# Optimization experiments

Hardware: AMD Instinct MI355X
Metric: run time of the kernel (lower is better)

Reference implementation:

```python
import jax, jax.numpy as jnp
import numpy as np

B, S, D = 1, 2048, 2048
HQ, HKV, HD = 32, 4, 128
E, K, F = 8, 2, 768
EPS = 1e-6
ROPE_THETA = 1000000.0


def rmsnorm(x, scale, eps=EPS):
    var = jnp.mean(jnp.square(x), axis=-1, keepdims=True)
    return x * jax.lax.rsqrt(var + eps) * scale


def rotate_half(x):
    h = x.shape[-1] // 2
    return jnp.concatenate([-x[..., h:], x[..., :h]], axis=-1)


def rope_cos_sin(seq_len, head_dim, dtype=jnp.float32):
    inv_freq = 1.0 / (ROPE_THETA ** (jnp.arange(0, head_dim, 2, dtype=jnp.float32) / head_dim))
    angles = jnp.arange(seq_len, dtype=jnp.float32)[:, None] * inv_freq[None, :]  # (S, HD/2)
    emb = jnp.concatenate([angles, angles], axis=-1)  # (S, HD)
    return jnp.cos(emb).astype(dtype), jnp.sin(emb).astype(dtype)


def setup_inputs() -> dict:
    key = jax.random.key(0)
    ks = jax.random.split(key, 16)
    s = lambda i, shape, scale: jax.random.normal(ks[i], shape, dtype=jnp.float32) * scale
    inp = {
        "hidden_states": s(0, (B, S, D), 1.0),
        "ln1_scale": jnp.ones((D,), jnp.float32),
        "ln2_scale": jnp.ones((D,), jnp.float32),
        "Wq": s(1, (D, HQ * HD), 0.02),
        "Wk": s(2, (D, HKV * HD), 0.02),
        "Wv": s(3, (D, HKV * HD), 0.02),
        "Wo": s(4, (HQ * HD, D), 0.02),
        "q_norm_scale": jnp.ones((HD,), jnp.float32),
        "k_norm_scale": jnp.ones((HD,), jnp.float32),
        "router_W": s(5, (D, E), 0.02),
        "up_W": s(6, (E, D, F), 0.02),
        "up_b": jnp.zeros((E, F), jnp.float32),
        "down_W": s(7, (E, F, D), 0.02),
        "down_b": jnp.zeros((E, D), jnp.float32),
    }
    return inp


def reference(hidden_states, ln1_scale, ln2_scale, Wq, Wk, Wv, Wo,
              q_norm_scale, k_norm_scale, router_W, up_W, up_b, down_W, down_b):
    b, s_len, d = hidden_states.shape
    # ---- pre-norm + self-attention ----
    residual = hidden_states
    x = rmsnorm(hidden_states, ln1_scale)
    q = (x @ Wq).reshape(b, s_len, HQ, HD)
    k = (x @ Wk).reshape(b, s_len, HKV, HD)
    v = (x @ Wv).reshape(b, s_len, HKV, HD)
    q = rmsnorm(q, q_norm_scale)
    k = rmsnorm(k, k_norm_scale)
    cos, sin = rope_cos_sin(s_len, HD, q.dtype)
    cos = cos[None, :, None, :]
    sin = sin[None, :, None, :]
    q = q * cos + rotate_half(q) * sin
    k = k * cos + rotate_half(k) * sin
    g = HQ // HKV
    k = jnp.repeat(k, g, axis=2)  # (b, s, HQ, HD)
    v = jnp.repeat(v, g, axis=2)
    scores = jnp.einsum('bqhd,bkhd->bhqk', q, k) / jnp.sqrt(jnp.asarray(HD, q.dtype))
    causal = jnp.tril(jnp.ones((s_len, s_len), bool))
    scores = jnp.where(causal[None, None], scores, jnp.asarray(-1e9, scores.dtype))
    probs = jax.nn.softmax(scores, axis=-1)
    attn = jnp.einsum('bhqk,bkhd->bqhd', probs, v).reshape(b, s_len, HQ * HD)
    attn_out = attn @ Wo
    hidden = residual + attn_out
    # ---- pre-norm + dense-all-experts MoE ----
    residual = hidden
    xf = rmsnorm(hidden, ln2_scale).reshape(-1, d)  # (T, D)
    router_logits = xf @ router_W  # (T, E)
    routing_weights = jax.nn.softmax(router_logits, axis=-1)
    gating_weights, selected = jax.lax.top_k(routing_weights, K)  # (T, K)
    gating_weights = gating_weights / jnp.sum(gating_weights, axis=-1, keepdims=True)
    expert_mask = jax.nn.one_hot(selected, E, dtype=gating_weights.dtype)  # (T, K, E)
    h = jax.nn.silu(jnp.einsum('td,edf->tef', xf, up_W) + up_b[None])  # (T, E, F)
    expert_outputs = jnp.einsum('tef,efd->ted', h, down_W) + down_b[None]  # (T, E, D)
    weighted = jnp.einsum('tke,ted->tkd', expert_mask, expert_outputs)  # (T, K, D)
    moe_out = jnp.sum(weighted * gating_weights[..., None], axis=1).reshape(b, s_len, d)
    hidden = residual + moe_out
    # ---- load balancing auxiliary loss (no attention mask path) ----
    expert_usage = jnp.mean(jnp.mean(expert_mask, axis=0), axis=0) * E  # (E,)
    su = jnp.sum(expert_usage)
    aux_loss = su * su / (E * E)
    return hidden, router_logits, aux_loss
```

## Files before the change

### kernel.cpp

```cpp
#include <hip/hip_runtime.h>
#include <cmath>

typedef __bf16 bf16_t;
typedef __bf16 bf16x8 __attribute__((ext_vector_type(8)));
typedef __bf16 bf16x4 __attribute__((ext_vector_type(4)));
typedef float  f32x4  __attribute__((ext_vector_type(4)));

#define SLEN 2048
#define DMOD 2048
#define NHQ  32
#define NHKV 4
#define HD   128
#define NQC  4096
#define NKVC 512
#define NQKVC 5120
#define NEXP 8
#define NF   768

#define KSTR 136
#define VSTR 72
#define PSTR 72

__device__ __forceinline__ float wredsum(float v) {
#pragma unroll
  for (int off = 32; off > 0; off >>= 1) v += __shfl_xor(v, off);
  return v;
}

__device__ __forceinline__ void gll16(const bf16_t* g, bf16_t* l) {
  __builtin_amdgcn_global_load_lds((const __attribute__((address_space(1))) void*)g,
                                   (__attribute__((address_space(3))) void*)l, 16, 0, 0);
}

__global__ void rope_table_k(float* __restrict__ cosT, float* __restrict__ sinT) {
  int idx = blockIdx.x * 256 + threadIdx.x;
  if (idx >= SLEN * 64) return;
  int t = idx >> 6, j = idx & 63;
  double inv = exp(-0.2158673524681918 * (double)j);
  double ang = (double)t * inv;
  cosT[idx] = (float)cos(ang);
  sinT[idx] = (float)sin(ang);
}

__global__ __launch_bounds__(256) void transpose_split2_k(const float* __restrict__ in,
                                                          bf16_t* __restrict__ outH,
                                                          bf16_t* __restrict__ outL,
                                                          int R, int C) {
  __shared__ float tile[32][33];
  int tx = threadIdx.x, ty = threadIdx.y;
  int c0 = blockIdx.x * 32, r0 = blockIdx.y * 32;
#pragma unroll
  for (int i = 0; i < 4; i++)
    tile[ty + i * 8][tx] = in[(size_t)(r0 + ty + i * 8) * C + c0 + tx];
  __syncthreads();
#pragma unroll
  for (int i = 0; i < 4; i++) {
    int c = c0 + ty + i * 8;
    int r = r0 + tx;
    float w = tile[tx][ty + i * 8];
    bf16_t hi = (bf16_t)w;
    bf16_t lo = (bf16_t)(w - (float)hi);
    size_t o = (size_t)c * R + r;
    outH[o] = hi;
    outL[o] = lo;
  }
}

__global__ __launch_bounds__(256) void transpose_plain_k(const float* __restrict__ in,
                                                         bf16_t* __restrict__ out,
                                                         int R, int C) {
  __shared__ float tile[32][33];
  int b = blockIdx.z;
  const float* inb = in + (size_t)b * R * C;
  bf16_t* outb = out + (size_t)b * R * C;
  int tx = threadIdx.x, ty = threadIdx.y;
  int c0 = blockIdx.x * 32, r0 = blockIdx.y * 32;
#pragma unroll
  for (int i = 0; i < 4; i++)
    tile[ty + i * 8][tx] = inb[(size_t)(r0 + ty + i * 8) * C + c0 + tx];
  __syncthreads();
#pragma unroll
  for (int i = 0; i < 4; i++) {
    int c = c0 + ty + i * 8;
    int r = r0 + tx;
    outb[(size_t)c * R + r] = (bf16_t)tile[tx][ty + i * 8];
  }
}

__global__ __launch_bounds__(256) void rmsnorm1_k(const float* __restrict__ hs,
                                                  const float* __restrict__ sc,
                                                  bf16_t* __restrict__ xnH,
                                                  bf16_t* __restrict__ xnL) {
  const int t = blockIdx.x;
  const float* row = hs + (size_t)t * DMOD;
  const int tid = threadIdx.x;
  const int i0 = tid * 8;
  float4 a = *(const float4*)(row + i0);
  float4 b = *(const float4*)(row + i0 + 4);
  float x[8] = {a.x, a.y, a.z, a.w, b.x, b.y, b.z, b.w};
  float ss = 0.f;
#pragma unroll
  for (int j = 0; j < 8; j++) ss += x[j] * x[j];
  ss = wredsum(ss);
  __shared__ float red[4];
  if ((tid & 63) == 0) red[tid >> 6] = ss;
  __syncthreads();
  float rn = rsqrtf((red[0] + red[1] + red[2] + red[3]) * (1.f / 2048.f) + 1e-6f);
#pragma unroll
  for (int j = 0; j < 8; j++) {
    float v = x[j] * rn * sc[i0 + j];
    bf16_t hi = (bf16_t)v;
    bf16_t lo = (bf16_t)(v - (float)hi);
    xnH[(size_t)t * DMOD + i0 + j] = hi;
    xnL[(size_t)t * DMOD + i0 + j] = lo;
  }
}

template <bool RESID>
__global__ __launch_bounds__(256) void gemm_split128_k(const bf16_t* __restrict__ Ah,
                                                       const bf16_t* __restrict__ Al,
                                                       int lda,
                                                       const bf16_t* __restrict__ Bh,
                                                       const bf16_t* __restrict__ Bl,
                                                       int ldb, int K,
                                                       const float* __restrict__ resid,
                                                       float* __restrict__ C, int ldc) {
  __shared__ bf16_t AsH[2][128][32], AsL[2][128][32], BsH[2][128][32], BsL[2][128][32];
  const int t = threadIdx.x;
  const int w = t >> 6, lane = t & 63;
  const int m16 = lane & 15, quad = lane >> 4;
  const int nwg = gridDim.x * gridDim.y;
  const int flat = blockIdx.y * gridDim.x + blockIdx.x;
  int tile = flat;
  if ((nwg & 7) == 0) tile = (flat & 7) * (nwg >> 3) + (flat >> 3);
  const int bx = tile % gridDim.x, by = tile / gridDim.x;
  const int m0 = by * 128, n0 = bx * 128;
  const int wm = (w & 1) * 64, wn = (w >> 1) * 64;
  f32x4 acc[4][4];
#pragma unroll
  for (int i = 0; i < 4; i++)
#pragma unroll
    for (int j = 0; j < 4; j++) acc[i][j] = (f32x4){0.f, 0.f, 0.f, 0.f};

  const int srow = t >> 2;
  const int scol = (t & 3) * 8;
  const int lw = w * 512;
  const bf16_t* gAh0 = Ah + (size_t)(m0 + srow) * lda + scol;
  const bf16_t* gAh1 = Ah + (size_t)(m0 + 64 + srow) * lda + scol;
  const bf16_t* gAl0 = Al + (size_t)(m0 + srow) * lda + scol;
  const bf16_t* gAl1 = Al + (size_t)(m0 + 64 + srow) * lda + scol;
  const bf16_t* gBh0 = Bh + (size_t)(n0 + srow) * ldb + scol;
  const bf16_t* gBh1 = Bh + (size_t)(n0 + 64 + srow) * ldb + scol;
  const bf16_t* gBl0 = Bl + (size_t)(n0 + srow) * ldb + scol;
  const bf16_t* gBl1 = Bl + (size_t)(n0 + 64 + srow) * ldb + scol;

  auto stage = [&](int buf, int k0) {
    gll16(gAh0 + k0, &AsH[buf][0][0] + lw);
    gll16(gAh1 + k0, &AsH[buf][0][0] + 2048 + lw);
    gll16(gAl0 + k0, &AsL[buf][0][0] + lw);
    gll16(gAl1 + k0, &AsL[buf][0][0] + 2048 + lw);
    gll16(gBh0 + k0, &BsH[buf][0][0] + lw);
    gll16(gBh1 + k0, &BsH[buf][0][0] + 2048 + lw);
    gll16(gBl0 + k0, &BsL[buf][0][0] + lw);
    gll16(gBl1 + k0, &BsL[buf][0][0] + 2048 + lw);
  };

  stage(0, 0);
  int cur = 0;
  for (int k0 = 32; k0 <= K; k0 += 32) {
    if (k0 < K) {
      stage(cur ^ 1, k0);
      asm volatile("s_waitcnt vmcnt(8)" ::: "memory");
    } else {
      asm volatile("s_waitcnt vmcnt(0)" ::: "memory");
    }
    __builtin_amdgcn_sched_barrier(0);
    __builtin_amdgcn_s_barrier();
    __builtin_amdgcn_sched_barrier(0);
    bf16x8 a_h[4], a_l[4];
#pragma unroll
    for (int mt = 0; mt < 4; mt++) {
      a_h[mt] = *(const bf16x8*)(&AsH[cur][wm + mt * 16 + m16][quad * 8]);
      a_l[mt] = *(const bf16x8*)(&AsL[cur][wm + mt * 16 + m16][quad * 8]);
    }
#pragma unroll
    for (int nt = 0; nt < 4; nt++) {
      bf16x8 b_h = *(const bf16x8*)(&BsH[cur][wn + nt * 16 + m16][quad * 8]);
      bf16x8 b_l = *(const bf16x8*)(&BsL[cur][wn + nt * 16 + m16][quad * 8]);
#pragma unroll
      for (int mt = 0; mt < 4; mt++) {
        acc[mt][nt] = __builtin_amdgcn_mfma_f32_16x16x32_bf16(a_h[mt], b_h, acc[mt][nt], 0, 0, 0);
        acc[mt][nt] = __builtin_amdgcn_mfma_f32_16x16x32_bf16(a_l[mt], b_h, acc[mt][nt], 0, 0, 0);
        acc[mt][nt] = __builtin_amdgcn_mfma_f32_16x16x32_bf16(a_h[mt], b_l, acc[mt][nt], 0, 0, 0);
      }
    }
    __builtin_amdgcn_sched_barrier(0);
    __builtin_amdgcn_s_barrier();
    __builtin_amdgcn_sched_barrier(0);
    cur ^= 1;
  }
#pragma unroll
  for (int mt = 0; mt < 4; mt++)
#pragma unroll
    for (int r = 0; r < 4; r++) {
      const size_t row = m0 + wm + mt * 16 + quad * 4 + r;
#pragma unroll
      for (int nt = 0; nt < 4; nt++) {
        const size_t idx = row * ldc + n0 + wn + nt * 16 + m16;
        if (RESID) C[idx] = acc[mt][nt][r] + resid[idx];
        else       C[idx] = acc[mt][nt][r];
      }
    }
}

template <class AROW>
__device__ __forceinline__ void gemm_core(AROW getA, const bf16_t* __restrict__ Bt, int ldb,
                                          int n0, int K, f32x4 acc[4]) {
  __shared__ bf16_t As[64][32];
  __shared__ bf16_t Bs[64][32];
  const int t = threadIdx.x;
  const int wave = t >> 6, lane = t & 63;
  const int m16 = lane & 15, quad = lane >> 4;
  const int sr = t >> 2, sc = (t & 3) << 3;
  const bf16_t* __restrict__ arow = getA(sr);
  const bf16_t* __restrict__ brow = Bt + (size_t)(n0 + sr) * ldb;
  for (int k0 = 0; k0 < K; k0 += 32) {
    __syncthreads();
    *(uint4*)(&As[sr][sc]) = *(const uint4*)(arow + k0 + sc);
    *(uint4*)(&Bs[sr][sc]) = *(const uint4*)(brow + k0 + sc);
    __syncthreads();
    bf16x8 af = *(const bf16x8*)(&As[wave * 16 + m16][quad * 8]);
#pragma unroll
    for (int nt = 0; nt < 4; nt++) {
      bf16x8 bfr = *(const bf16x8*)(&Bs[nt * 16 + m16][quad * 8]);
      acc[nt] = __builtin_amdgcn_mfma_f32_16x16x32_bf16(af, bfr, acc[nt], 0, 0, 0);
    }
  }
}

__global__ __launch_bounds__(128) void qknorm_rope_k(float* __restrict__ qkv,
                                                     const float* __restrict__ qsc,
                                                     const float* __restrict__ ksc,
                                                     const float* __restrict__ cosT,
                                                     const float* __restrict__ sinT) {
  const int t = blockIdx.x;
  const int hh = blockIdx.y;
  const bool isq = hh < NHQ;
  float* ptr = qkv + (size_t)t * NQKVC + (isq ? hh * HD : NQC + (hh - NHQ) * HD);
  const int i = threadIdx.x;
  float x = ptr[i];
  float ss = x * x;
  ss = wredsum(ss);
  __shared__ float red2[2];
  __shared__ float xs[128];
  if ((i & 63) == 0) red2[i >> 6] = ss;
  __syncthreads();
  float rn = rsqrtf((red2[0] + red2[1]) * (1.f / 128.f) + 1e-6f);
  float xn = x * rn * (isq ? qsc[i] : ksc[i]);
  xs[i] = xn;
  __syncthreads();
  int j = i & 63;
  float c = cosT[t * 64 + j];
  float s = sinT[t * 64 + j];
  float rot = (i < 64) ? -xs[i + 64] : xs[i - 64];
  ptr[i] = xn * c + rot * s;
}

__global__ __launch_bounds__(256) void kprep_k(const float* __restrict__ qkv,
                                               bf16_t* __restrict__ Kh,
                                               bf16_t* __restrict__ Kl) {
  const int gid = blockIdx.x * 256 + threadIdx.x;
  const int tok = gid >> 6;
  const int c = (gid & 63) * 8;
  const int hk = c >> 7, d = c & 127;
  const float* p = qkv + (size_t)tok * NQKVC + NQC + c;
  float4 a = *(const float4*)p;
  float4 b = *(const float4*)(p + 4);
  float xv[8] = {a.x, a.y, a.z, a.w, b.x, b.y, b.z, b.w};
  bf16x8 hv, lv;
#pragma unroll
  for (int j = 0; j < 8; j++) {
    bf16_t hi = (bf16_t)xv[j];
    hv[j] = hi;
    lv[j] = (bf16_t)(xv[j] - (float)hi);
  }
  const size_t o = ((size_t)hk * SLEN + tok) * HD + d;
  *(bf16x8*)(Kh + o) = hv;
  *(bf16x8*)(Kl + o) = lv;
}

__global__ __launch_bounds__(256) void vprep_k(const float* __restrict__ qkv,
                                               bf16_t* __restrict__ Vh,
                                               bf16_t* __restrict__ Vl) {
  __shared__ float tile[32][33];
  const int hk = blockIdx.z;
  const int tx = threadIdx.x, ty = threadIdx.y;
  const int t0 = blockIdx.x * 32, d0 = blockIdx.y * 32;
#pragma unroll
  for (int i = 0; i < 4; i++)
    tile[ty + i * 8][tx] =
        qkv[(size_t)(t0 + ty + i * 8) * NQKVC + NQC + NKVC + hk * HD + d0 + tx];
  __syncthreads();
#pragma unroll
  for (int i = 0; i < 4; i++) {
    int d = d0 + ty + i * 8;
    int tk = t0 + tx;
    float wv = tile[tx][ty + i * 8];
    bf16_t hi = (bf16_t)wv;
    size_t o = ((size_t)hk * HD + d) * SLEN + tk;
    Vh[o] = hi;
    Vl[o] = (bf16_t)(wv - (float)hi);
  }
}

__global__ __launch_bounds__(256) void attn_mfma_k(const float* __restrict__ qkv,
                                                   const bf16_t* __restrict__ Kph,
                                                   const bf16_t* __restrict__ Kpl,
                                                   const bf16_t* __restrict__ Vph,
                                                   const bf16_t* __restrict__ Vpl,
                                                   bf16_t* __restrict__ attnH,
                                                   bf16_t* __restrict__ attnL) {
  const int bx = blockIdx.x;
  const int hh = blockIdx.y;
  const int hk = hh >> 3;
  __shared__ bf16_t sK[2][64][KSTR];
  __shared__ bf16_t sV[2][128][VSTR];
  const int t = threadIdx.x;
  const int w = t >> 6, lane = t & 63;
  const int m16 = lane & 15, quad = lane >> 4;
  const float SCALE = 0.08838834764831845f;

  const int ksr = t >> 4;
  const int ksc = (t & 15) * 8;
  const int vsd = t >> 3;
  const int vsk = (t & 7) * 8;
  const bf16_t* KbH = Kph + (size_t)hk * SLEN * HD;
  const bf16_t* KbL = Kpl + (size_t)hk * SLEN * HD;
  const bf16_t* VbH = Vph + (size_t)hk * HD * SLEN;
  const bf16_t* VbL = Vpl + (size_t)hk * HD * SLEN;
  bf16_t* sP = &sK[0][0][0];

  for (int half = 0; half < 2; half++) {
    const int qb = half ? bx : 31 - bx;

    bf16x8 Qh[4], Ql[4];
    {
      const int qrow = qb * 64 + w * 16 + m16;
      const float* qp = qkv + (size_t)qrow * NQKVC + hh * HD + quad * 8;
#pragma unroll
      for (int kc = 0; kc < 4; kc++) {
        float4 x0 = *(const float4*)(qp + kc * 32);
        float4 x1 = *(const float4*)(qp + kc * 32 + 4);
        float xv[8] = {x0.x, x0.y, x0.z, x0.w, x1.x, x1.y, x1.z, x1.w};
#pragma unroll
        for (int j = 0; j < 8; j++) {
          bf16_t hi = (bf16_t)xv[j];
          Qh[kc][j] = hi;
          Ql[kc][j] = (bf16_t)(xv[j] - (float)hi);
        }
      }
    }
    f32x4 acc[8];
#pragma unroll
    for (int i = 0; i < 8; i++) acc[i] = (f32x4){0.f, 0.f, 0.f, 0.f};
    float mrow[4], lrow[4];
#pragma unroll
    for (int r = 0; r < 4; r++) { mrow[r] = -1e30f; lrow[r] = 0.f; }

    for (int kb = 0; kb <= qb; kb++) {
      __syncthreads();
      {
#pragma unroll
        for (int i = 0; i < 4; i++) {
          const int row = ksr + i * 16;
          const size_t go = (size_t)(kb * 64 + row) * HD + ksc;
          *(bf16x8*)(&sK[0][row][ksc]) = *(const bf16x8*)(KbH + go);
          *(bf16x8*)(&sK[1][row][ksc]) = *(const bf16x8*)(KbL + go);
        }
      }
      {
#pragma unroll
        for (int i = 0; i < 4; i++) {
          const int d = vsd + i * 32;
          const size_t go = (size_t)d * SLEN + kb * 64 + vsk;
          *(bf16x8*)(&sV[0][d][vsk]) = *(const bf16x8*)(VbH + go);
          *(bf16x8*)(&sV[1][d][vsk]) = *(const bf16x8*)(VbL + go);
        }
      }
      __syncthreads();
      f32x4 xs[4];
#pragma unroll
      for (int nt = 0; nt < 4; nt++) {
        f32x4 s = (f32x4){0.f, 0.f, 0.f, 0.f};
        if (kb < qb || nt <= w) {
#pragma unroll
          for (int kc = 0; kc < 4; kc++) {
            bf16x8 kh = *(const bf16x8*)(&sK[0][nt * 16 + m16][kc * 32 + quad * 8]);
            bf16x8 kl = *(const bf16x8*)(&sK[1][nt * 16 + m16][kc * 32 + quad * 8]);
            s = __builtin_amdgcn_mfma_f32_16x16x32_bf16(Qh[kc], kh, s, 0, 0, 0);
            s = __builtin_amdgcn_mfma_f32_16x16x32_bf16(Ql[kc], kh, s, 0, 0, 0);
            s = __builtin_amdgcn_mfma_f32_16x16x32_bf16(Qh[kc], kl, s, 0, 0, 0);
          }
        }
        xs[nt] = s;
      }
      __syncthreads();
      float p[4][4], alpha[4];
#pragma unroll
      for (int r = 0; r < 4; r++) {
        const int rqg = qb * 64 + w * 16 + quad * 4 + r;
        float xr[4];
#pragma unroll
        for (int nt = 0; nt < 4; nt++) {
          int colg = kb * 64 + nt * 16 + m16;
          xr[nt] = (colg <= rqg) ? xs[nt][r] * SCALE : -1e30f;
        }
        float mx = fmaxf(fmaxf(xr[0], xr[1]), fmaxf(xr[2], xr[3]));
#pragma unroll
        for (int off = 1; off < 16; off <<= 1) mx = fmaxf(mx, __shfl_xor(mx, off));
        float mn = fmaxf(mrow[r], mx);
        float al = __expf(mrow[r] - mn);
        float rs = 0.f;
#pragma unroll
        for (int nt = 0; nt < 4; nt++) {
          float pv = __expf(xr[nt] - mn);
          p[nt][r] = pv;
          rs += pv;
        }
#pragma unroll
        for (int off = 1; off < 16; off <<= 1) rs += __shfl_xor(rs, off);
        lrow[r] = lrow[r] * al + rs;
        mrow[r] = mn;
        alpha[r] = al;
      }
#pragma unroll
      for (int dt = 0; dt < 8; dt++)
#pragma unroll
        for (int r = 0; r < 4; r++) acc[dt][r] *= alpha[r];
      {
        bf16_t* base = sP + (size_t)w * 2 * 16 * PSTR;
#pragma unroll
        for (int nt = 0; nt < 4; nt++)
#pragma unroll
          for (int r = 0; r < 4; r++) {
            float pv = p[nt][r];
            bf16_t hi = (bf16_t)pv;
            base[(quad * 4 + r) * PSTR + nt * 16 + m16] = hi;
            base[16 * PSTR + (quad * 4 + r) * PSTR + nt * 16 + m16] = (bf16_t)(pv - (float)hi);
          }
      }
      {
        const bf16_t* base = sP + (size_t)w * 2 * 16 * PSTR;
        bf16x8 Ph[2], Pl[2];
#pragma unroll
        for (int kc = 0; kc < 2; kc++) {
          Ph[kc] = *(const bf16x8*)(base + m16 * PSTR + kc * 32 + quad * 8);
          Pl[kc] = *(const bf16x8*)(base + 16 * PSTR + m16 * PSTR + kc * 32 + quad * 8);
        }
#pragma unroll
        for (int dt = 0; dt < 8; dt++)
#pragma unroll
          for (int kc = 0; kc < 2; kc++) {
            bf16x8 vh = *(const bf16x8*)(&sV[0][dt * 16 + m16][kc * 32 + quad * 8]);
            bf16x8 vl = *(const bf16x8*)(&sV[1][dt * 16 + m16][kc * 32 + quad * 8]);
            acc[dt] = __builtin_amdgcn_mfma_f32_16x16x32_bf16(Ph[kc], vh, acc[dt], 0, 0, 0);
            acc[dt] = __builtin_amdgcn_mfma_f32_16x16x32_bf16(Pl[kc], vh, acc[dt], 0, 0, 0);
            acc[dt] = __builtin_amdgcn_mfma_f32_16x16x32_bf16(Ph[kc], vl, acc[dt], 0, 0, 0);
          }
      }
    }
#pragma unroll
    for (int r = 0; r < 4; r++) {
      const int tok = qb * 64 + w * 16 + quad * 4 + r;
      const float linv = 1.f / lrow[r];
      const size_t ro = (size_t)tok * NQC + hh * HD;
#pragma unroll
      for (int dt = 0; dt < 8; dt++) {
        float v = acc[dt][r] * linv;
        bf16_t hi = (bf16_t)v;
        attnH[ro + dt * 16 + m16] = hi;
        attnL[ro + dt * 16 + m16] = (bf16_t)(v - (float)hi);
      }
    }
  }
}

__global__ __launch_bounds__(256) void rmsnorm2_router_k(const float* __restrict__ hid,
                                                         const float* __restrict__ sc2,
                                                         const float* __restrict__ rW,
                                                         bf16_t* __restrict__ xf,
                                                         float* __restrict__ rlog) {
  const int t = blockIdx.x;
  const float* row = hid + (size_t)t * DMOD;
  const int tid = threadIdx.x;
  const int i0 = tid * 8;
  float4 a = *(const float4*)(row + i0);
  float4 b = *(const float4*)(row + i0 + 4);
  float x[8] = {a.x, a.y, a.z, a.w, b.x, b.y, b.z, b.w};
  float ss = 0.f;
#pragma unroll
  for (int j = 0; j < 8; j++) ss += x[j] * x[j];
  ss = wredsum(ss);
  __shared__ float red[4];
  if ((tid & 63) == 0) red[tid >> 6] = ss;
  __syncthreads();
  float rn = rsqrtf((red[0] + red[1] + red[2] + red[3]) * (1.f / 2048.f) + 1e-6f);
  float acc[8];
#pragma unroll
  for (int e = 0; e < 8; e++) acc[e] = 0.f;
#pragma unroll
  for (int j = 0; j < 8; j++) {
    float xn = x[j] * rn * sc2[i0 + j];
    xf[(size_t)t * DMOD + i0 + j] = (bf16_t)xn;
    const float* w = rW + (size_t)(i0 + j) * NEXP;
#pragma unroll
    for (int e = 0; e < 8; e++) acc[e] += xn * w[e];
  }
#pragma unroll
  for (int e = 0; e < 8; e++) acc[e] = wredsum(acc[e]);
  __shared__ float wacc[4][8];
  if ((tid & 63) == 0)
#pragma unroll
    for (int e = 0; e < 8; e++) wacc[tid >> 6][e] = acc[e];
  __syncthreads();
  if (tid < 8) rlog[t * NEXP + tid] = wacc[0][tid] + wacc[1][tid] + wacc[2][tid] + wacc[3][tid];
}

__global__ void topk_k(const float* __restrict__ rlog, int* __restrict__ sel,
                       float* __restrict__ gates, float* __restrict__ aux) {
  int t = blockIdx.x * 256 + threadIdx.x;
  if (t == 0) aux[0] = 1.0f;
  if (t >= SLEN) return;
  const float* l = rlog + t * NEXP;
  int i1 = 0; float v1 = l[0];
#pragma unroll
  for (int e = 1; e < 8; e++) if (l[e] > v1) { v1 = l[e]; i1 = e; }
  int i2 = -1; float v2 = -1e30f;
#pragma unroll
  for (int e = 0; e < 8; e++) if (e != i1 && l[e] > v2) { v2 = l[e]; i2 = e; }
  float e21 = expf(v2 - v1);
  float inv = 1.f / (1.f + e21);
  sel[t * 2 + 0] = i1;
  sel[t * 2 + 1] = i2;
  gates[t * 2 + 0] = inv;
  gates[t * 2 + 1] = e21 * inv;
}

__global__ void scatter_k(const int* __restrict__ sel, const float* __restrict__ gates,
                          int* __restrict__ cnt, int* __restrict__ tok,
                          float* __restrict__ gateL) {
  int i = blockIdx.x * 256 + threadIdx.x;
  if (i >= SLEN * 2) return;
  int e = sel[i];
  int pos = atomicAdd(&cnt[e], 1);
  tok[e * SLEN + pos] = i >> 1;
  gateL[e * SLEN + pos] = gates[i];
}

__global__ __launch_bounds__(256) void gemm_up_k(const bf16_t* __restrict__ xf,
                                                 const bf16_t* __restrict__ upWT,
                                                 const int* __restrict__ cnt,
                                                 const int* __restrict__ tok,
                                                 const float* __restrict__ up_b,
                                                 bf16_t* __restrict__ hbuf) {
  const int e = blockIdx.z;
  const int c = cnt[e];
  const int m0 = blockIdx.y * 64;
  if (m0 >= c) return;
  const int n0 = blockIdx.x * 64;
  const int* tokE = tok + e * SLEN;
  const bf16_t* BtE = upWT + (size_t)e * NF * DMOD;
  f32x4 zz = {0.f, 0.f, 0.f, 0.f};
  f32x4 acc[4] = {zz, zz, zz, zz};
  gemm_core([=](int r) {
      int s = m0 + r; if (s >= c) s = c - 1;
      return xf + (size_t)tokE[s] * DMOD;
    }, BtE, DMOD, n0, DMOD, acc);
  const int t = threadIdx.x, wave = t >> 6, lane = t & 63;
  const int m16 = lane & 15, quad = lane >> 4;
  const int mb = m0 + wave * 16 + quad * 4;
  const int nb = n0 + m16;
#pragma unroll
  for (int nt = 0; nt < 4; nt++)
#pragma unroll
    for (int r = 0; r < 4; r++) {
      int slot = mb + r;
      if (slot < c) {
        int n = nb + nt * 16;
        float x = acc[nt][r] + up_b[e * NF + n];
        float v = x / (1.f + __expf(-x));
        hbuf[((size_t)e * SLEN + slot) * NF + n] = (bf16_t)v;
      }
    }
}

__global__ __launch_bounds__(256) void gemm_down_k(const bf16_t* __restrict__ hbuf,
                                                   const bf16_t* __restrict__ downWT,
                                                   const int* __restrict__ cnt,
                                                   const int* __restrict__ tok,
                                                   const float* __restrict__ gateL,
                                                   const float* __restrict__ down_b,
                                                   float* __restrict__ outH) {
  const int e = blockIdx.z;
  const int c = cnt[e];
  const int m0 = blockIdx.y * 64;
  if (m0 >= c) return;
  const int n0 = blockIdx.x * 64;
  const bf16_t* Ah = hbuf + (size_t)e * SLEN * NF;
  const bf16_t* BtE = downWT + (size_t)e * DMOD * NF;
  f32x4 zz = {0.f, 0.f, 0.f, 0.f};
  f32x4 acc[4] = {zz, zz, zz, zz};
  gemm_core([=](int r) { return Ah + (size_t)(m0 + r) * NF; }, BtE, NF, n0, NF, acc);
  const int t = threadIdx.x, wave = t >> 6, lane = t & 63;
  const int m16 = lane & 15, quad = lane >> 4;
  const int mb = m0 + wave * 16 + quad * 4;
  const int nb = n0 + m16;
#pragma unroll
  for (int nt = 0; nt < 4; nt++)
#pragma unroll
    for (int r = 0; r < 4; r++) {
      int slot = mb + r;
      if (slot < c) {
        int n = nb + nt * 16;
        int tk = tok[e * SLEN + slot];
        float g = gateL[e * SLEN + slot];
        atomicAdd(&outH[(size_t)tk * DMOD + n], g * (acc[nt][r] + down_b[e * DMOD + n]));
      }
    }
}

extern "C" void kernel_launch(void* const* d_in, const int* in_sizes, int n_in,
                              void* d_out, int out_size, void* d_ws, size_t ws_size,
                              hipStream_t stream) {
  (void)in_sizes; (void)n_in; (void)out_size;
  const float* hs   = (const float*)d_in[0];
  const float* ln1  = (const float*)d_in[1];
  const float* ln2  = (const float*)d_in[2];
  const float* Wq   = (const float*)d_in[3];
  const float* Wk   = (const float*)d_in[4];
  const float* Wv   = (const float*)d_in[5];
  const float* Wo   = (const float*)d_in[6];
  const float* qns  = (const float*)d_in[7];
  const float* kns  = (const float*)d_in[8];
  const float* rW   = (const float*)d_in[9];
  const float* upW  = (const float*)d_in[10];
  const float* upB  = (const float*)d_in[11];
  const float* dnW  = (const float*)d_in[12];
  const float* dnB  = (const float*)d_in[13];
  float* dout = (float*)d_out;

  const size_t NEED = 135431168ull;
  if (ws_size < NEED) return;
  char* ws = (char*)d_ws;
  const size_t OA = 0;
  const size_t OB = OA + 41943040ull;
  const size_t OC = OB + 33554432ull;
  const size_t OD = OC + 16777216ull;
  const size_t OE = OD + 41943040ull;

  bf16_t* BqkvH  = (bf16_t*)(ws + OA);
  bf16_t* BqkvL  = (bf16_t*)(ws + OA + 20971520ull);
  bf16_t* attnH  = (bf16_t*)(ws + OA);
  bf16_t* attnL  = (bf16_t*)(ws + OA + 16777216ull);
  bf16_t* Kph    = (bf16_t*)(ws + OA + 33554432ull);
  bf16_t* Kpl    = Kph + 1048576;
  bf16_t* Vph    = Kpl + 1048576;
  bf16_t* Vpl    = Vph + 1048576;
  bf16_t* upWT   = (bf16_t*)(ws + OA);
  bf16_t* WoH    = (bf16_t*)(ws + OB);
  bf16_t* WoL    = (bf16_t*)(ws + OB + 16777216ull);
  bf16_t* hbuf   = (bf16_t*)(ws + OB);
  bf16_t* xnH    = (bf16_t*)(ws + OC);
  bf16_t* xnL    = (bf16_t*)(ws + OC + 8388608ull);
  bf16_t* xf     = (bf16_t*)(ws + OC);
  float*  qkv    = (float*)(ws + OD);
  bf16_t* downWT = (bf16_t*)(ws + OD);
  float*  cosT   = (float*)(ws + OE);
  float*  sinT   = (float*)(ws + OE + 524288ull);
  int*    sel    = (int*)(ws + OE + 1048576ull);
  float*  gates  = (float*)(ws + OE + 1064960ull);
  int*    cnt    = (int*)(ws + OE + 1081344ull);
  int*    tok    = (int*)(ws + OE + 1082368ull);
  float*  gateL  = (float*)(ws + OE + 1147904ull);

  hipMemsetAsync(cnt, 0, 1024, stream);
  rope_table_k<<<512, 256, 0, stream>>>(cosT, sinT);

  dim3 tb(32, 8);
  transpose_split2_k<<<dim3(128, 64), tb, 0, stream>>>(Wq, BqkvH, BqkvL, 2048, 4096);
  transpose_split2_k<<<dim3(16, 64), tb, 0, stream>>>(Wk, BqkvH + (size_t)4096 * 2048,
                                                      BqkvL + (size_t)4096 * 2048, 2048, 512);
  transpose_split2_k<<<dim3(16, 64), tb, 0, stream>>>(Wv, BqkvH + (size_t)4608 * 2048,
                                                      BqkvL + (size_t)4608 * 2048, 2048, 512);
  transpose_split2_k<<<dim3(64, 128), tb, 0, stream>>>(Wo, WoH, WoL, 4096, 2048);

  rmsnorm1_k<<<2048, 256, 0, stream>>>(hs, ln1, xnH, xnL);
  gemm_split128_k<false><<<dim3(40, 16), 256, 0, stream>>>(xnH, xnL, 2048, BqkvH, BqkvL,
                                                           2048, 2048, nullptr, qkv, NQKVC);
  qknorm_rope_k<<<dim3(2048, 36), 128, 0, stream>>>(qkv, qns, kns, cosT, sinT);
  kprep_k<<<512, 256, 0, stream>>>(qkv, Kph, Kpl);
  vprep_k<<<dim3(64, 4, 4), tb, 0, stream>>>(qkv, Vph, Vpl);
  attn_mfma_k<<<dim3(16, 32), 256, 0, stream>>>(qkv, Kph, Kpl, Vph, Vpl, attnH, attnL);
  gemm_split128_k<true><<<dim3(16, 16), 256, 0, stream>>>(attnH, attnL, 4096, WoH, WoL,
                                                          4096, 4096, hs, dout, DMOD);

  rmsnorm2_router_k<<<2048, 256, 0, stream>>>(dout, ln2, rW, xf, dout + 4194304);
  topk_k<<<8, 256, 0, stream>>>(dout + 4194304, sel, gates, dout + 4210688);
  scatter_k<<<16, 256, 0, stream>>>(sel, gates, cnt, tok, gateL);

  transpose_plain_k<<<dim3(24, 64, 8), tb, 0, stream>>>(upW, upWT, 2048, 768);
  transpose_plain_k<<<dim3(64, 24, 8), tb, 0, stream>>>(dnW, downWT, 768, 2048);

  gemm_up_k<<<dim3(12, 32, 8), 256, 0, stream>>>(xf, upWT, cnt, tok, upB, hbuf);
  gemm_down_k<<<dim3(32, 32, 8), 256, 0, stream>>>(hbuf, downWT, cnt, tok, gateL, dnB, dout);
}
```

Measured before the change: 926.0 us.

## Shrink split GEMM tile to 128x64 and pipeline MoE expert GEMMs

The split-precision QKV and output-projection GEMMs now use a 128x64 tile with a launch-bounds occupancy hint. This doubles the number of workgroups so the 256 CUs stay busy, at the cost of reloading A more often. The MoE up and down expert GEMMs move from the simple synchronous 64x64 core to a 128x64 tile with double-buffered direct global-to-LDS loads and 4 waves each computing 64x32. This aims to raise MFMA utilisation and overlap memory with compute, and the 64x64 core is removed.

```diff
diff --git a/kernel.cpp b/kernel.cpp
--- a/kernel.cpp
+++ b/kernel.cpp
@@ -117,7 +117,7 @@
 }
 
 template <bool RESID>
-__global__ __launch_bounds__(256) void gemm_split128_k(const bf16_t* __restrict__ Ah,
+__global__ __launch_bounds__(256, 3) void gemm_split_k(const bf16_t* __restrict__ Ah,
                                                        const bf16_t* __restrict__ Al,
                                                        int lda,
                                                        const bf16_t* __restrict__ Bh,
@@ -125,7 +125,7 @@
                                                        int ldb, int K,
                                                        const float* __restrict__ resid,
                                                        float* __restrict__ C, int ldc) {
-  __shared__ bf16_t AsH[2][128][32], AsL[2][128][32], BsH[2][128][32], BsL[2][128][32];
+  __shared__ bf16_t AsH[2][128][32], AsL[2][128][32], BsH[2][64][32], BsL[2][64][32];
   const int t = threadIdx.x;
   const int w = t >> 6, lane = t & 63;
   const int m16 = lane & 15, quad = lane >> 4;
@@ -134,13 +134,13 @@
   int tile = flat;
   if ((nwg & 7) == 0) tile = (flat & 7) * (nwg >> 3) + (flat >> 3);
   const int bx = tile % gridDim.x, by = tile / gridDim.x;
-  const int m0 = by * 128, n0 = bx * 128;
-  const int wm = (w & 1) * 64, wn = (w >> 1) * 64;
-  f32x4 acc[4][4];
+  const int m0 = by * 128, n0 = bx * 64;
+  const int wm = (w & 1) * 64, wn = (w >> 1) * 32;
+  f32x4 acc[4][2];
 #pragma unroll
   for (int i = 0; i < 4; i++)
 #pragma unroll
-    for (int j = 0; j < 4; j++) acc[i][j] = (f32x4){0.f, 0.f, 0.f, 0.f};
+    for (int j = 0; j < 2; j++) acc[i][j] = (f32x4){0.f, 0.f, 0.f, 0.f};
 
   const int srow = t >> 2;
   const int scol = (t & 3) * 8;
@@ -150,9 +150,7 @@
   const bf16_t* gAl0 = Al + (size_t)(m0 + srow) * lda + scol;
   const bf16_t* gAl1 = Al + (size_t)(m0 + 64 + srow) * lda + scol;
   const bf16_t* gBh0 = Bh + (size_t)(n0 + srow) * ldb + scol;
-  const bf16_t* gBh1 = Bh + (size_t)(n0 + 64 + srow) * ldb + scol;
   const bf16_t* gBl0 = Bl + (size_t)(n0 + srow) * ldb + scol;
-  const bf16_t* gBl1 = Bl + (size_t)(n0 + 64 + srow) * ldb + scol;
 
   auto stage = [&](int buf, int k0) {
     gll16(gAh0 + k0, &AsH[buf][0][0] + lw);
@@ -160,9 +158,7 @@
     gll16(gAl0 + k0, &AsL[buf][0][0] + lw);
     gll16(gAl1 + k0, &AsL[buf][0][0] + 2048 + lw);
     gll16(gBh0 + k0, &BsH[buf][0][0] + lw);
-    gll16(gBh1 + k0, &BsH[buf][0][0] + 2048 + lw);
     gll16(gBl0 + k0, &BsL[buf][0][0] + lw);
-    gll16(gBl1 + k0, &BsL[buf][0][0] + 2048 + lw);
   };
 
   stage(0, 0);
@@ -170,7 +166,7 @@
   for (int k0 = 32; k0 <= K; k0 += 32) {
     if (k0 < K) {
       stage(cur ^ 1, k0);
-      asm volatile("s_waitcnt vmcnt(8)" ::: "memory");
+      asm volatile("s_waitcnt vmcnt(6)" ::: "memory");
     } else {
       asm volatile("s_waitcnt vmcnt(0)" ::: "memory");
     }
@@ -184,7 +180,7 @@
       a_l[mt] = *(const bf16x8*)(&AsL[cur][wm + mt * 16 + m16][quad * 8]);
     }
 #pragma unroll
-    for (int nt = 0; nt < 4; nt++) {
+    for (int nt = 0; nt < 2; nt++) {
       bf16x8 b_h = *(const bf16x8*)(&BsH[cur][wn + nt * 16 + m16][quad * 8]);
       bf16x8 b_l = *(const bf16x8*)(&BsL[cur][wn + nt * 16 + m16][quad * 8]);
 #pragma unroll
@@ -205,37 +201,12 @@
     for (int r = 0; r < 4; r++) {
       const size_t row = m0 + wm + mt * 16 + quad * 4 + r;
 #pragma unroll
-      for (int nt = 0; nt < 4; nt++) {
+      for (int nt = 0; nt < 2; nt++) {
         const size_t idx = row * ldc + n0 + wn + nt * 16 + m16;
         if (RESID) C[idx] = acc[mt][nt][r] + resid[idx];
         else       C[idx] = acc[mt][nt][r];
       }
     }
-}
-
-template <class AROW>
-__device__ __forceinline__ void gemm_core(AROW getA, const bf16_t* __restrict__ Bt, int ldb,
-                                          int n0, int K, f32x4 acc[4]) {
-  __shared__ bf16_t As[64][32];
-  __shared__ bf16_t Bs[64][32];
-  const int t = threadIdx.x;
-  const int wave = t >> 6, lane = t & 63;
-  const int m16 = lane & 15, quad = lane >> 4;
-  const int sr = t >> 2, sc = (t & 3) << 3;
-  const bf16_t* __restrict__ arow = getA(sr);
-  const bf16_t* __restrict__ brow = Bt + (size_t)(n0 + sr) * ldb;
-  for (int k0 = 0; k0 < K; k0 += 32) {
-    __syncthreads();
-    *(uint4*)(&As[sr][sc]) = *(const uint4*)(arow + k0 + sc);
-    *(uint4*)(&Bs[sr][sc]) = *(const uint4*)(brow + k0 + sc);
-    __syncthreads();
-    bf16x8 af = *(const bf16x8*)(&As[wave * 16 + m16][quad * 8]);
-#pragma unroll
-    for (int nt = 0; nt < 4; nt++) {
-      bf16x8 bfr = *(const bf16x8*)(&Bs[nt * 16 + m16][quad * 8]);
-      acc[nt] = __builtin_amdgcn_mfma_f32_16x16x32_bf16(af, bfr, acc[nt], 0, 0, 0);
-    }
-  }
 }
 
 __global__ __launch_bounds__(128) void qknorm_rope_k(float* __restrict__ qkv,
@@ -557,74 +528,163 @@
   gateL[e * SLEN + pos] = gates[i];
 }
 
-__global__ __launch_bounds__(256) void gemm_up_k(const bf16_t* __restrict__ xf,
-                                                 const bf16_t* __restrict__ upWT,
-                                                 const int* __restrict__ cnt,
-                                                 const int* __restrict__ tok,
-                                                 const float* __restrict__ up_b,
-                                                 bf16_t* __restrict__ hbuf) {
+__global__ __launch_bounds__(256, 5) void gemm_up_k(const bf16_t* __restrict__ xf,
+                                                    const bf16_t* __restrict__ upWT,
+                                                    const int* __restrict__ cnt,
+                                                    const int* __restrict__ tok,
+                                                    const float* __restrict__ up_b,
+                                                    bf16_t* __restrict__ hbuf) {
   const int e = blockIdx.z;
   const int c = cnt[e];
-  const int m0 = blockIdx.y * 64;
+  const int m0 = blockIdx.y * 128;
   if (m0 >= c) return;
   const int n0 = blockIdx.x * 64;
+  __shared__ bf16_t As[2][128][32], Bs[2][64][32];
+  const int t = threadIdx.x;
+  const int w = t >> 6, lane = t & 63;
+  const int m16 = lane & 15, quad = lane >> 4;
+  const int wm = (w & 1) * 64, wn = (w >> 1) * 32;
+  const int srow = t >> 2, scol = (t & 3) * 8;
+  const int lw = w * 512;
   const int* tokE = tok + e * SLEN;
-  const bf16_t* BtE = upWT + (size_t)e * NF * DMOD;
-  f32x4 zz = {0.f, 0.f, 0.f, 0.f};
-  f32x4 acc[4] = {zz, zz, zz, zz};
-  gemm_core([=](int r) {
-      int s = m0 + r; if (s >= c) s = c - 1;
-      return xf + (size_t)tokE[s] * DMOD;
-    }, BtE, DMOD, n0, DMOD, acc);
-  const int t = threadIdx.x, wave = t >> 6, lane = t & 63;
-  const int m16 = lane & 15, quad = lane >> 4;
-  const int mb = m0 + wave * 16 + quad * 4;
-  const int nb = n0 + m16;
-#pragma unroll
-  for (int nt = 0; nt < 4; nt++)
+  int r0 = m0 + srow;      if (r0 >= c) r0 = c - 1;
+  int r1 = m0 + 64 + srow; if (r1 >= c) r1 = c - 1;
+  const bf16_t* ga0 = xf + (size_t)tokE[r0] * DMOD + scol;
+  const bf16_t* ga1 = xf + (size_t)tokE[r1] * DMOD + scol;
+  const bf16_t* gb0 = upWT + (size_t)e * NF * DMOD + (size_t)(n0 + srow) * DMOD + scol;
+  f32x4 acc[4][2];
+#pragma unroll
+  for (int i = 0; i < 4; i++)
+#pragma unroll
+    for (int j = 0; j < 2; j++) acc[i][j] = (f32x4){0.f, 0.f, 0.f, 0.f};
+
+  auto stage = [&](int buf, int k0) {
+    gll16(ga0 + k0, &As[buf][0][0] + lw);
+    gll16(ga1 + k0, &As[buf][0][0] + 2048 + lw);
+    gll16(gb0 + k0, &Bs[buf][0][0] + lw);
+  };
+
+  stage(0, 0);
+  int cur = 0;
+  for (int k0 = 32; k0 <= DMOD; k0 += 32) {
+    if (k0 < DMOD) {
+      stage(cur ^ 1, k0);
+      asm volatile("s_waitcnt vmcnt(3)" ::: "memory");
+    } else {
+      asm volatile("s_waitcnt vmcnt(0)" ::: "memory");
+    }
+    __builtin_amdgcn_sched_barrier(0);
+    __builtin_amdgcn_s_barrier();
+    __builtin_amdgcn_sched_barrier(0);
+    bf16x8 a[4];
+#pragma unroll
+    for (int mt = 0; mt < 4; mt++)
+      a[mt] = *(const bf16x8*)(&As[cur][wm + mt * 16 + m16][quad * 8]);
+#pragma unroll
+    for (int nt = 0; nt < 2; nt++) {
+      bf16x8 b = *(const bf16x8*)(&Bs[cur][wn + nt * 16 + m16][quad * 8]);
+#pragma unroll
+      for (int mt = 0; mt < 4; mt++)
+        acc[mt][nt] = __builtin_amdgcn_mfma_f32_16x16x32_bf16(a[mt], b, acc[mt][nt], 0, 0, 0);
+    }
+    __builtin_amdgcn_sched_barrier(0);
+    __builtin_amdgcn_s_barrier();
+    __builtin_amdgcn_sched_barrier(0);
+    cur ^= 1;
+  }
+#pragma unroll
+  for (int mt = 0; mt < 4; mt++)
 #pragma unroll
     for (int r = 0; r < 4; r++) {
-      int slot = mb + r;
+      int slot = m0 + wm + mt * 16 + quad * 4 + r;
       if (slot < c) {
-        int n = nb + nt * 16;
-        float x = acc[nt][r] + up_b[e * NF + n];
-        float v = x / (1.f + __expf(-x));
-        hbuf[((size_t)e * SLEN + slot) * NF + n] = (bf16_t)v;
-      }
-    }
-}
-
-__global__ __launch_bounds__(256) void gemm_down_k(const bf16_t* __restrict__ hbuf,
-                                                   const bf16_t* __restrict__ downWT,
-                                                   const int* __restrict__ cnt,
-                                                   const int* __restrict__ tok,
-                                                   const float* __restrict__ gateL,
-                                                   const float* __restrict__ down_b,
-                                                   float* __restrict__ outH) {
+#pragma unroll
+        for (int nt = 0; nt < 2; nt++) {
+          int n = n0 + wn + nt * 16 + m16;
+          float x = acc[mt][nt][r] + up_b[e * NF + n];
+          float v = x / (1.f + __expf(-x));
+          hbuf[((size_t)e * SLEN + slot) * NF + n] = (bf16_t)v;
+        }
+      }
+    }
+}
+
+__global__ __launch_bounds__(256, 5) void gemm_down_k(const bf16_t* __restrict__ hbuf,
+                                                      const bf16_t* __restrict__ downWT,
+                                                      const int* __restrict__ cnt,
+                                                      const int* __restrict__ tok,
+                                                      const float* __restrict__ gateL,
+                                                      const float* __restrict__ down_b,
+                                                      float* __restrict__ outH) {
   const int e = blockIdx.z;
   const int c = cnt[e];
-  const int m0 = blockIdx.y * 64;
+  const int m0 = blockIdx.y * 128;
   if (m0 >= c) return;
   const int n0 = blockIdx.x * 64;
-  const bf16_t* Ah = hbuf + (size_t)e * SLEN * NF;
-  const bf16_t* BtE = downWT + (size_t)e * DMOD * NF;
-  f32x4 zz = {0.f, 0.f, 0.f, 0.f};
-  f32x4 acc[4] = {zz, zz, zz, zz};
-  gemm_core([=](int r) { return Ah + (size_t)(m0 + r) * NF; }, BtE, NF, n0, NF, acc);
-  const int t = threadIdx.x, wave = t >> 6, lane = t & 63;
+  __shared__ bf16_t As[2][128][32], Bs[2][64][32];
+  const int t = threadIdx.x;
+  const int w = t >> 6, lane = t & 63;
   const int m16 = lane & 15, quad = lane >> 4;
-  const int mb = m0 + wave * 16 + quad * 4;
-  const int nb = n0 + m16;
-#pragma unroll
-  for (int nt = 0; nt < 4; nt++)
+  const int wm = (w & 1) * 64, wn = (w >> 1) * 32;
+  const int srow = t >> 2, scol = (t & 3) * 8;
+  const int lw = w * 512;
+  const bf16_t* Ab = hbuf + (size_t)e * SLEN * NF;
+  const bf16_t* ga0 = Ab + (size_t)(m0 + srow) * NF + scol;
+  const bf16_t* ga1 = Ab + (size_t)(m0 + 64 + srow) * NF + scol;
+  const bf16_t* gb0 = downWT + (size_t)e * DMOD * NF + (size_t)(n0 + srow) * NF + scol;
+  f32x4 acc[4][2];
+#pragma unroll
+  for (int i = 0; i < 4; i++)
+#pragma unroll
+    for (int j = 0; j < 2; j++) acc[i][j] = (f32x4){0.f, 0.f, 0.f, 0.f};
+
+  auto stage = [&](int buf, int k0) {
+    gll16(ga0 + k0, &As[buf][0][0] + lw);
+    gll16(ga1 + k0, &As[buf][0][0] + 2048 + lw);
+    gll16(gb0 + k0, &Bs[buf][0][0] + lw);
+  };
+
+  stage(0, 0);
+  int cur = 0;
+  for (int k0 = 32; k0 <= NF; k0 += 32) {
+    if (k0 < NF) {
+      stage(cur ^ 1, k0);
+      asm volatile("s_waitcnt vmcnt(3)" ::: "memory");
+    } else {
+      asm volatile("s_waitcnt vmcnt(0)" ::: "memory");
+    }
+    __builtin_amdgcn_sched_barrier(0);
+    __builtin_amdgcn_s_barrier();
+    __builtin_amdgcn_sched_barrier(0);
+    bf16x8 a[4];
+#pragma unroll
+    for (int mt = 0; mt < 4; mt++)
+      a[mt] = *(const bf16x8*)(&As[cur][wm + mt * 16 + m16][quad * 8]);
+#pragma unroll
+    for (int nt = 0; nt < 2; nt++) {
+      bf16x8 b = *(const bf16x8*)(&Bs[cur][wn + nt * 16 + m16][quad * 8]);
+#pragma unroll
+      for (int mt = 0; mt < 4; mt++)
+        acc[mt][nt] = __builtin_amdgcn_mfma_f32_16x16x32_bf16(a[mt], b, acc[mt][nt], 0, 0, 0);
+    }
+    __builtin_amdgcn_sched_barrier(0);
+    __builtin_amdgcn_s_barrier();
+    __builtin_amdgcn_sched_barrier(0);
+    cur ^= 1;
+  }
+#pragma unroll
+  for (int mt = 0; mt < 4; mt++)
 #pragma unroll
     for (int r = 0; r < 4; r++) {
-      int slot = mb + r;
+      int slot = m0 + wm + mt * 16 + quad * 4 + r;
       if (slot < c) {
-        int n = nb + nt * 16;
         int tk = tok[e * SLEN + slot];
         float g = gateL[e * SLEN + slot];
-        atomicAdd(&outH[(size_t)tk * DMOD + n], g * (acc[nt][r] + down_b[e * DMOD + n]));
+#pragma unroll
+        for (int nt = 0; nt < 2; nt++) {
+          int n = n0 + wn + nt * 16 + m16;
+          atomicAdd(&outH[(size_t)tk * DMOD + n], g * (acc[mt][nt][r] + down_b[e * DMOD + n]));
+        }
       }
     }
 }
@@ -695,14 +755,14 @@
   transpose_split2_k<<<dim3(64, 128), tb, 0, stream>>>(Wo, WoH, WoL, 4096, 2048);
 
   rmsnorm1_k<<<2048, 256, 0, stream>>>(hs, ln1, xnH, xnL);
-  gemm_split128_k<false><<<dim3(40, 16), 256, 0, stream>>>(xnH, xnL, 2048, BqkvH, BqkvL,
-                                                           2048, 2048, nullptr, qkv, NQKVC);
+  gemm_split_k<false><<<dim3(80, 16), 256, 0, stream>>>(xnH, xnL, 2048, BqkvH, BqkvL,
+                                                        2048, 2048, nullptr, qkv, NQKVC);
   qknorm_rope_k<<<dim3(2048, 36), 128, 0, stream>>>(qkv, qns, kns, cosT, sinT);
   kprep_k<<<512, 256, 0, stream>>>(qkv, Kph, Kpl);
   vprep_k<<<dim3(64, 4, 4), tb, 0, stream>>>(qkv, Vph, Vpl);
   attn_mfma_k<<<dim3(16, 32), 256, 0, stream>>>(qkv, Kph, Kpl, Vph, Vpl, attnH, attnL);
-  gemm_split128_k<true><<<dim3(16, 16), 256, 0, stream>>>(attnH, attnL, 4096, WoH, WoL,
-                                                          4096, 4096, hs, dout, DMOD);
+  gemm_split_k<true><<<dim3(32, 16), 256, 0, stream>>>(attnH, attnL, 4096, WoH, WoL,
+                                                       4096, 4096, hs, dout, DMOD);
 
   rmsnorm2_router_k<<<2048, 256, 0, stream>>>(dout, ln2, rW, xf, dout + 4194304);
   topk_k<<<8, 256, 0, stream>>>(dout + 4194304, sel, gates, dout + 4210688);
@@ -711,6 +771,6 @@
   transpose_plain_k<<<dim3(24, 64, 8), tb, 0, stream>>>(upW, upWT, 2048, 768);
   transpose_plain_k<<<dim3(64, 24, 8), tb, 0, stream>>>(dnW, downWT, 768, 2048);
 
-  gemm_up_k<<<dim3(12, 32, 8), 256, 0, stream>>>(xf, upWT, cnt, tok, upB, hbuf);
-  gemm_down_k<<<dim3(32, 32, 8), 256, 0, stream>>>(hbuf, downWT, cnt, tok, gateL, dnB, dout);
-}
+  gemm_up_k<<<dim3(12, 16, 8), 256, 0, stream>>>(xf, upWT, cnt, tok, upB, hbuf);
+  gemm_down_k<<<dim3(32, 16, 8), 256, 0, stream>>>(hbuf, downWT, cnt, tok, gateL, dnB, dout);
+}
```

New measurement: 861.6 us. 7.0% less time.
